# Kernel tuning notes

Measured on AMD Instinct MI355X. Metric: run time of the kernel, lower is better.

Reference implementation:

```python
import jax, jax.numpy as jnp
import numpy as np

# dims derived from init_kwargs
B, C, T, F = 16, 2, 16, 256
TP, FP = 4, 4            # time/freq patch
MF = F // FP             # 64 freq tokens
TIC = T // TP            # 4 time tokens per chunk
S = MF * TIC             # 256 tokens per chunk
CTX = 3
LEFT = S * CTX           # 768 cached tokens
MT = TIC * (CTX + 1)     # 16 max time positions
D, H, G = 512, 8, 4      # d_model, q heads, kv groups
HD = D // H              # 64
R = H // G               # 2 q-heads per kv group
L = 4                    # layers
FFH = 4 * D
EPS = 1e-5


def _ln(x, g, b):
    m = jnp.mean(x, -1, keepdims=True)
    v = jnp.mean((x - m) ** 2, -1, keepdims=True)
    return (x - m) * jax.lax.rsqrt(v + EPS) * g + b


def setup_inputs() -> dict:
    key = jax.random.key(0)
    ks = iter(jax.random.split(key, 20))
    rn = lambda shape, s=0.05: jax.random.normal(next(ks), shape, jnp.float32) * s
    return {
        "x": rn((B, C, T, F), 1.0),
        "cache_k": rn((L, B, G, LEFT, HD), 1.0),
        "cache_v": rn((L, B, G, LEFT, HD), 1.0),
        "in_W": rn((TP * FP * C, D)), "in_b": jnp.zeros((D,)),
        "ln1_g": jnp.ones((L, D)), "ln1_b": jnp.zeros((L, D)),
        "Wq": rn((L, D, D)), "bq": jnp.zeros((L, D)),
        "Wk": rn((L, D, G * HD)), "bk": jnp.zeros((L, G * HD)),
        "Wv": rn((L, D, G * HD)), "bv": jnp.zeros((L, G * HD)),
        "Wo": rn((L, D, D)), "bo": jnp.zeros((L, D)),
        "rel_time": rn((L, 2 * MT - 1, H)), "rel_freq": rn((L, 2 * MF - 1, H)),
        "res_a": jnp.ones((L,)),
        "ln2_g": jnp.ones((L, D)), "ln2_b": jnp.zeros((L, D)),
        "W1": rn((L, D, FFH)), "b1": jnp.zeros((L, FFH)),
        "W3": rn((L, D, FFH)), "b3": jnp.zeros((L, FFH)),
        "W2": rn((L, FFH, D)), "b2": jnp.zeros((L, D)),
        "res_f": jnp.ones((L,)),
        "out_W": rn((D, TP * FP * C)), "out_b": jnp.zeros((TP * FP * C,)),
    }


def reference(x, cache_k, cache_v, in_W, in_b, ln1_g, ln1_b, Wq, bq, Wk, bk, Wv, bv,
              Wo, bo, rel_time, rel_freq, res_a, ln2_g, ln2_b, W1, b1, W3, b3, W2, b2,
              res_f, out_W, out_b):
    # patchify: (B,C,T,F) -> (B, S, TP*FP*C), token order time-major / freq inner
    h = jnp.transpose(x, (0, 2, 3, 1)).reshape(B, TIC, TP, MF, FP, C)
    h = jnp.transpose(h, (0, 1, 3, 2, 4, 5)).reshape(B, S, TP * FP * C)
    h = h @ in_W + in_b  # (B,S,D)

    # 2D relative position indices (identical each layer)
    K = LEFT + S
    q_idx = jnp.arange(S)
    k_idx = jnp.arange(K)
    qt = LEFT // MF + q_idx // MF  # query time = cache time offset + local time
    qf = q_idx % MF
    kt = k_idx // MF
    kf = k_idx % MF
    dt = qt[:, None] - kt[None, :] + (MT - 1)  # (S,K) in [0, 2*MT-2]
    df = qf[:, None] - kf[None, :] + (MF - 1)  # (S,K) in [0, 2*MF-2]
    scale = 1.0 / np.sqrt(HD).astype(np.float32)

    new_ck, new_cv = [], []
    for l in range(L):
        # --- streaming GQA attention with 2D rel-pos and KV cache ---
        xin = _ln(h, ln1_g[l], ln1_b[l])
        q = (xin @ Wq[l] + bq[l]).reshape(B, S, H, HD)
        k = (xin @ Wk[l] + bk[l]).reshape(B, S, G, HD)
        v = (xin @ Wv[l] + bv[l]).reshape(B, S, G, HD)
        k_full = jnp.concatenate([cache_k[l], jnp.transpose(k, (0, 2, 1, 3))], axis=2)  # (B,G,K,HD)
        v_full = jnp.concatenate([cache_v[l], jnp.transpose(v, (0, 2, 1, 3))], axis=2)
        new_ck.append(k_full[:, :, -LEFT:])
        new_cv.append(v_full[:, :, -LEFT:])
        # group q heads: head h -> group h // R
        scores = jnp.einsum('bsgrd,bgtd->bgrst', q.reshape(B, S, G, R, HD), k_full) * scale
        bias = rel_time[l][dt] + rel_freq[l][df]          # (S,K,H)
        bias = jnp.transpose(bias, (2, 0, 1)).reshape(G, R, S, K)
        attn = jax.nn.softmax(scores + bias[None], axis=-1)
        o = jnp.einsum('bgrst,bgtd->bsgrd', attn, v_full).reshape(B, S, D)
        o = o @ Wo[l] + bo[l]
        h = h + res_a[l] * o  # dropout/droppath identity at eval
        # --- SwiGLU FFN ---
        xin = _ln(h, ln2_g[l], ln2_b[l])
        ff = (jax.nn.silu(xin @ W1[l] + b1[l]) * (xin @ W3[l] + b3[l])) @ W2[l] + b2[l]
        h = h + res_f[l] * ff

    y = h @ out_W + out_b  # (B,S,TP*FP*C)
    # unpatchify back to (B,C,T,F)
    y = y.reshape(B, TIC, MF, TP, FP, C)
    y = jnp.transpose(y, (0, 1, 3, 2, 4, 5)).reshape(B, T, F, C)
    y = jnp.transpose(y, (0, 3, 1, 2))
    return y, jnp.stack(new_ck), jnp.stack(new_cv)
```

## Files before the change

### kernel.cpp

```cpp
#include <hip/hip_runtime.h>
#include <stdint.h>

typedef __attribute__((ext_vector_type(8))) short bf16x8;
typedef __attribute__((ext_vector_type(4))) float f32x4;

#define B_    16
#define S_    256
#define LEFT_ 768
#define KT_   1024
#define D_    512
#define H_    8
#define G_    4
#define HD_   64
#define L_    4
#define FFH_  2048
#define M_    4096
#define LOG2E 1.44269504f

__device__ __forceinline__ unsigned short f2b(float f){
  unsigned u = __float_as_uint(f);
  u += 0x7fffu + ((u>>16)&1u);
  return (unsigned short)(u>>16);
}

__device__ __forceinline__ void gl_lds16(const unsigned short* g, void* l){
  __builtin_amdgcn_global_load_lds(
    (const __attribute__((address_space(1))) unsigned int*)g,
    (__attribute__((address_space(3))) unsigned int*)l, 16, 0, 0);
}

template<int BM, int BN, int WM, int WN, class BRowF>
__device__ __forceinline__ void mfma_core(
    const unsigned short* Abase, int lda, int m0, BRowF brow,
    int kd, char* As, char* Bs, f32x4* acc)
{
  constexpr int FR = WM/16, FC = WN/16;
  constexpr int NWC = BN/WN;
  constexpr int CA = BM/64, CB = BN/64;
  const int tid = threadIdx.x, wave = tid>>6, lane = tid&63;
  const int wr = wave / NWC, wc = wave % NWC;
  const int lr = lane>>2;
  const int swl = (lane&3) ^ ((lane>>2)&3) ^ (lane>>4);

  auto stage = [&](int buf, int k0){
    #pragma unroll
    for (int i = 0; i < CA; ++i) {
      const int chunk = wave*CA + i;
      const unsigned short* gp = Abase + (size_t)(m0 + chunk*16 + lr)*lda + k0 + swl*8;
      gl_lds16(gp, As + buf*(BM*64) + chunk*1024);
    }
    #pragma unroll
    for (int i = 0; i < CB; ++i) {
      const int chunk = wave*CB + i;
      const unsigned short* gp = brow(chunk*16 + lr) + k0 + swl*8;
      gl_lds16(gp, Bs + buf*(BN*64) + chunk*1024);
    }
  };

  stage(0, 0);
  __syncthreads();
  int cur = 0;
  for (int k0 = 0; k0 < kd; k0 += 32) {
    if (k0 + 32 < kd) stage(cur^1, k0 + 32);
    bf16x8 af[FR], bfr[FC];
    #pragma unroll
    for (int r = 0; r < FR; ++r)
      af[r] = *(const bf16x8*)(As + cur*(BM*64) + (wr*WM + r*16 + (lane&15))*64 + swl*16);
    #pragma unroll
    for (int c = 0; c < FC; ++c)
      bfr[c] = *(const bf16x8*)(Bs + cur*(BN*64) + (wc*WN + c*16 + (lane&15))*64 + swl*16);
    #pragma unroll
    for (int r = 0; r < FR; ++r)
      #pragma unroll
      for (int c = 0; c < FC; ++c)
        acc[r*FC+c] = __builtin_amdgcn_mfma_f32_16x16x32_bf16(af[r], bfr[c], acc[r*FC+c], 0, 0, 0);
    __syncthreads();
    cur ^= 1;
  }
}

__device__ __forceinline__ void tcvt_body(
    const float* __restrict__ src, unsigned short* __restrict__ dst,
    int K, int N, int ntk, int ntn, int bx)
{
  __shared__ float t[64][65];
  int kt = bx % ntk; int nt = (bx/ntk) % ntn; int l = bx/(ntk*ntn);
  src += (size_t)l*K*N; dst += (size_t)l*N*K;
  const int k0 = kt*64, n0 = nt*64;
  const int tid = threadIdx.x;
  #pragma unroll
  for (int i = 0; i < 4; ++i) {
    int kr = (tid>>4) + i*16;
    const float4 v = *(const float4*)&src[(size_t)(k0+kr)*N + n0 + (tid&15)*4];
    t[kr][(tid&15)*4+0]=v.x; t[kr][(tid&15)*4+1]=v.y;
    t[kr][(tid&15)*4+2]=v.z; t[kr][(tid&15)*4+3]=v.w;
  }
  __syncthreads();
  const int nn = tid>>2, kk = (tid&3)*16;
  unsigned w[8];
  #pragma unroll
  for (int j = 0; j < 8; ++j)
    w[j] = (unsigned)f2b(t[kk+2*j][nn]) | ((unsigned)f2b(t[kk+2*j+1][nn])<<16);
  size_t off = (size_t)(n0+nn)*K + k0 + kk;
  *(uint4*)&dst[off]     = make_uint4(w[0],w[1],w[2],w[3]);
  *(uint4*)&dst[off + 8] = make_uint4(w[4],w[5],w[6],w[7]);
}

__global__ __launch_bounds__(256) void transpose_all(
    const float* __restrict__ Wq, const float* __restrict__ Wk,
    const float* __restrict__ Wv, const float* __restrict__ Wo,
    const float* __restrict__ W1, const float* __restrict__ W3,
    const float* __restrict__ W2,
    unsigned short* __restrict__ Wqt, unsigned short* __restrict__ Wkt,
    unsigned short* __restrict__ Wvt, unsigned short* __restrict__ Wot,
    unsigned short* __restrict__ W1t, unsigned short* __restrict__ W3t,
    unsigned short* __restrict__ W2t)
{
  int bx = blockIdx.x;
  if      (bx < 256)  tcvt_body(Wq, Wqt, 512, 512, 8, 8,  bx);
  else if (bx < 384)  tcvt_body(Wk, Wkt, 512, 256, 8, 4,  bx-256);
  else if (bx < 512)  tcvt_body(Wv, Wvt, 512, 256, 8, 4,  bx-384);
  else if (bx < 768)  tcvt_body(Wo, Wot, 512, 512, 8, 8,  bx-512);
  else if (bx < 1792) tcvt_body(W1, W1t, 512, 2048, 8, 32, bx-768);
  else if (bx < 2816) tcvt_body(W3, W3t, 512, 2048, 8, 32, bx-1792);
  else                tcvt_body(W2, W2t, 2048, 512, 32, 8, bx-2816);
}

__global__ __launch_bounds__(256) void patchify_inproj(
    const float* __restrict__ x, const float* __restrict__ inW,
    const float* __restrict__ inb, float* __restrict__ h)
{
  __shared__ float wlds[32*512];
  __shared__ float ps[16][33];
  const int tid = threadIdx.x;
  const int tb = blockIdx.x*16;

  #pragma unroll
  for (int i = 0; i < 16; ++i)
    ((float4*)wlds)[i*256 + tid] = ((const float4*)inW)[i*256 + tid];
  {
    int tok = tid >> 5, idx = tid & 31;
    int bs = tb + tok;
    int b = bs >> 8, s = bs & 255;
    int tic = s >> 6, mf = s & 63;
    int tp = idx >> 3, fp = (idx >> 1) & 3, c = idx & 1;
    ps[tok][idx] = x[((size_t)(b*2 + c)*16 + tic*4 + tp)*256 + mf*4 + fp];
    int tok2 = tok + 8;
    int bs2 = tb + tok2;
    int b2 = bs2 >> 8, s2 = bs2 & 255;
    int tic2 = s2 >> 6, mf2 = s2 & 63;
    ps[tok2][idx] = x[((size_t)(b2*2 + c)*16 + tic2*4 + tp)*256 + mf2*4 + fp];
  }
  __syncthreads();

  const int g = tid >> 4, qd = tid & 15;
  const int bs = tb + g;
  for (int j = 0; j < 32; ++j) {
    int d = j*16 + qd;
    float acc = inb[d];
    #pragma unroll
    for (int i = 0; i < 32; ++i) acc += ps[g][i] * wlds[i*512 + d];
    h[(size_t)bs*512 + d] = acc;
  }
}

__global__ __launch_bounds__(256) void ln_stats(
    const float* __restrict__ h, float* __restrict__ smean, float* __restrict__ srstd)
{
  const int tid = threadIdx.x;
  const int row = blockIdx.x*16 + (tid>>4);
  const int qd = tid & 15;
  const float* rp = h + (size_t)row*512 + qd*32;
  float s = 0.f, sq = 0.f;
  #pragma unroll
  for (int i = 0; i < 8; ++i) {
    float4 v = ((const float4*)rp)[i];
    s  += (v.x+v.y)+(v.z+v.w);
    sq += (v.x*v.x+v.y*v.y)+(v.z*v.z+v.w*v.w);
  }
  #pragma unroll
  for (int o = 1; o < 16; o <<= 1) { s += __shfl_xor(s,o,64); sq += __shfl_xor(sq,o,64); }
  if (qd == 0) {
    float mean = s*(1.f/512.f);
    smean[row] = mean;
    srstd[row] = rsqrtf(sq*(1.f/512.f) - mean*mean + 1e-5f);
  }
}

__global__ __launch_bounds__(256) void ln_kernel(
    const float* __restrict__ in, unsigned short* __restrict__ out,
    const float* __restrict__ g, const float* __restrict__ bta)
{
  const int tid = threadIdx.x;
  const int row = blockIdx.x*16 + (tid>>4);
  const int qd = tid & 15;
  const float* rp = in + (size_t)row*512 + qd*32;
  float4 xv[8];
  float s = 0.f, sq = 0.f;
  #pragma unroll
  for (int i = 0; i < 8; ++i) {
    xv[i] = ((const float4*)rp)[i];
    s  += (xv[i].x+xv[i].y)+(xv[i].z+xv[i].w);
    sq += (xv[i].x*xv[i].x + xv[i].y*xv[i].y)+(xv[i].z*xv[i].z + xv[i].w*xv[i].w);
  }
  #pragma unroll
  for (int o = 1; o < 16; o <<= 1) { s += __shfl_xor(s,o,64); sq += __shfl_xor(sq,o,64); }
  const float mean = s*(1.f/512.f);
  const float rstd = rsqrtf(sq*(1.f/512.f) - mean*mean + 1e-5f);
  const float* gp = g + qd*32;
  const float* bp = bta + qd*32;
  unsigned short* op = out + (size_t)row*512 + qd*32;
  #pragma unroll
  for (int i = 0; i < 4; ++i) {
    float4 a  = xv[2*i],                 b2 = xv[2*i+1];
    float4 ga = ((const float4*)gp)[2*i], gb = ((const float4*)gp)[2*i+1];
    float4 ba = ((const float4*)bp)[2*i], bb = ((const float4*)bp)[2*i+1];
    unsigned w0 = (unsigned)f2b((a.x-mean)*rstd*ga.x + ba.x) | ((unsigned)f2b((a.y-mean)*rstd*ga.y + ba.y)<<16);
    unsigned w1 = (unsigned)f2b((a.z-mean)*rstd*ga.z + ba.z) | ((unsigned)f2b((a.w-mean)*rstd*ga.w + ba.w)<<16);
    unsigned w2 = (unsigned)f2b((b2.x-mean)*rstd*gb.x + bb.x) | ((unsigned)f2b((b2.y-mean)*rstd*gb.y + bb.y)<<16);
    unsigned w3 = (unsigned)f2b((b2.z-mean)*rstd*gb.z + bb.z) | ((unsigned)f2b((b2.w-mean)*rstd*gb.w + bb.w)<<16);
    *(uint4*)(op + i*8) = make_uint4(w0,w1,w2,w3);
  }
}

__global__ __launch_bounds__(256) void qkv_ln_gemm(
    const float* __restrict__ h,
    const float* __restrict__ smean, const float* __restrict__ srstd,
    const float* __restrict__ lng, const float* __restrict__ lnb,
    const unsigned short* __restrict__ Wqt, const unsigned short* __restrict__ Wkt,
    const unsigned short* __restrict__ Wvt,
    const float* __restrict__ bq, const float* __restrict__ bk_, const float* __restrict__ bv_,
    unsigned short* __restrict__ q_bf, unsigned short* __restrict__ kf_bf,
    unsigned short* __restrict__ vnew, float* __restrict__ nck, float* __restrict__ ncv)
{
  __shared__ alignas(16) char As[2][64*64];
  __shared__ alignas(16) char Bs[2][128*64];
  int bx = (blockIdx.x & 7)*64 + (blockIdx.x >> 3);
  const int mt = bx >> 3, nt = bx & 7;
  const int m0 = mt*64, n0 = nt*128;
  const int tid = threadIdx.x, wave = tid>>6, lane = tid&63;

  const int ar = tid >> 2, au = tid & 3;
  const int ap = au ^ (ar&3) ^ ((ar>>2)&3);
  const float* arow = h + (size_t)(m0 + ar)*512;
  const float mean_r = smean[m0 + ar];
  const float rstd_r = srstd[m0 + ar];

  const int lr = lane>>2;
  const int swl = (lane&3) ^ ((lane>>2)&3) ^ (lane>>4);
  auto brow = [&](int rr) -> const unsigned short* {
    int n = n0 + rr;
    return n < 512 ? Wqt + (size_t)n*512
         : n < 768 ? Wkt + (size_t)(n-512)*512
                   : Wvt + (size_t)(n-768)*512;
  };
  auto stageB = [&](int buf, int k0){
    #pragma unroll
    for (int i = 0; i < 2; ++i) {
      const int chunk = wave*2 + i;
      gl_lds16(brow(chunk*16+lr) + k0 + swl*8, (char*)Bs[buf] + chunk*1024);
    }
  };

  float4 av[6];
  auto loadA = [&](int k0){
    av[0] = *(const float4*)(arow + k0 + au*8);
    av[1] = *(const float4*)(arow + k0 + au*8 + 4);
    av[2] = *(const float4*)(lng  + k0 + au*8);
    av[3] = *(const float4*)(lng  + k0 + au*8 + 4);
    av[4] = *(const float4*)(lnb  + k0 + au*8);
    av[5] = *(const float4*)(lnb  + k0 + au*8 + 4);
  };
  auto writeA = [&](int buf){
    const float* xv = (const float*)&av[0];
    const float* gv = (const float*)&av[2];
    const float* bv2 = (const float*)&av[4];
    unsigned w[4];
    #pragma unroll
    for (int j = 0; j < 4; ++j) {
      float e0 = (xv[2*j]   - mean_r)*rstd_r*gv[2*j]   + bv2[2*j];
      float e1 = (xv[2*j+1] - mean_r)*rstd_r*gv[2*j+1] + bv2[2*j+1];
      w[j] = (unsigned)f2b(e0) | ((unsigned)f2b(e1)<<16);
    }
    *(uint4*)((char*)As[buf] + ar*64 + ap*16) = make_uint4(w[0],w[1],w[2],w[3]);
  };

  loadA(0);
  stageB(0, 0);
  writeA(0);
  __syncthreads();

  f32x4 acc[8] = {};
  const int wr = wave >> 1, wc = wave & 1;
  for (int k0 = 0; k0 < 512; k0 += 32) {
    const int cur = (k0>>5)&1;
    const bool more = (k0 + 32 < 512);
    if (more) { stageB(cur^1, k0+32); loadA(k0+32); }
    bf16x8 af[2], bfv[4];
    #pragma unroll
    for (int r = 0; r < 2; ++r)
      af[r] = *(const bf16x8*)((char*)As[cur] + (wr*32 + r*16 + (lane&15))*64 + swl*16);
    #pragma unroll
    for (int c = 0; c < 4; ++c)
      bfv[c] = *(const bf16x8*)((char*)Bs[cur] + (wc*64 + c*16 + (lane&15))*64 + swl*16);
    #pragma unroll
    for (int r = 0; r < 2; ++r)
      #pragma unroll
      for (int c = 0; c < 4; ++c)
        acc[r*4+c] = __builtin_amdgcn_mfma_f32_16x16x32_bf16(af[r], bfv[c], acc[r*4+c], 0,0,0);
    if (more) writeA(cur^1);
    __syncthreads();
  }

  #pragma unroll
  for (int r = 0; r < 2; ++r)
  #pragma unroll
  for (int c = 0; c < 4; ++c) {
    f32x4 v = acc[r*4+c];
    #pragma unroll
    for (int reg = 0; reg < 4; ++reg) {
      int m = m0 + wr*32 + r*16 + ((lane>>4)<<2) + reg;
      int n = n0 + wc*64 + c*16 + (lane&15);
      float val = v[reg];
      int b = m >> 8, s = m & 255;
      if (n < 512) {
        q_bf[(size_t)m*512 + n] = f2b(val + bq[n]);
      } else if (n < 768) {
        int g = (n-512) >> 6, hd = n & 63;
        float kv = val + bk_[n-512];
        kf_bf[((size_t)(b*4+g)*1024 + 768 + s)*64 + hd] = f2b(kv);
        nck [((size_t)(b*4+g)*768  + 512 + s)*64 + hd] = kv;
      } else {
        int g = (n-768) >> 6, hd = n & 63;
        float vv = val + bv_[n-768];
        vnew[(size_t)m*256 + (n-768)] = f2b(vv);
        ncv [((size_t)(b*4+g)*768 + 512 + s)*64 + hd] = vv;
      }
    }
  }
}

__global__ __launch_bounds__(256) void merge_kv(
    const float* __restrict__ ck, const float* __restrict__ cv,
    const unsigned short* __restrict__ vnew,
    unsigned short* __restrict__ kf_bf, unsigned short* __restrict__ vt_bf,
    float* __restrict__ nck, float* __restrict__ ncv)
{
  __shared__ float t[64][65];
  const int bb = blockIdx.x;
  const int tid = threadIdx.x;
  if (bb < 3072) {
    size_t idx = (size_t)bb*256 + tid;
    int hd4 = idx & 15;
    size_t tt = (idx >> 4) % 768;
    size_t bg = idx / (16*768);
    const float4 v = ((const float4*)ck)[idx];
    uint2 pk;
    pk.x = (unsigned)f2b(v.x) | ((unsigned)f2b(v.y)<<16);
    pk.y = (unsigned)f2b(v.z) | ((unsigned)f2b(v.w)<<16);
    *(uint2*)&kf_bf[((bg*1024 + tt)*64) + hd4*4] = pk;
    if (tt >= 256)
      ((float4*)nck)[(bg*768 + (tt-256))*16 + hd4] = v;
  } else if (bb < 3840) {
    const int bi = bb - 3072;
    const int bg = bi / 12, tt = bi % 12;
    const int t0 = tt*64;
    #pragma unroll
    for (int i = 0; i < 4; ++i) {
      int tr = (tid>>4) + i*16;
      const float4 v = ((const float4*)cv)[((size_t)bg*768 + t0+tr)*16 + (tid&15)];
      t[tr][(tid&15)*4+0]=v.x; t[tr][(tid&15)*4+1]=v.y;
      t[tr][(tid&15)*4+2]=v.z; t[tr][(tid&15)*4+3]=v.w;
      if (t0+tr >= 256)
        ((float4*)ncv)[((size_t)bg*768 + t0+tr-256)*16 + (tid&15)] = v;
    }
    __syncthreads();
    const int hd = tid>>2, tc = (tid&3)*16;
    unsigned w[8];
    #pragma unroll
    for (int j = 0; j < 8; ++j)
      w[j] = (unsigned)f2b(t[tc+2*j][hd]) | ((unsigned)f2b(t[tc+2*j+1][hd])<<16);
    size_t off = ((size_t)bg*64 + hd)*1024 + t0 + tc;
    *(uint4*)&vt_bf[off]     = make_uint4(w[0],w[1],w[2],w[3]);
    *(uint4*)&vt_bf[off + 8] = make_uint4(w[4],w[5],w[6],w[7]);
  } else {
    const int bi = bb - 3840;
    const int bg = bi >> 2, tt4 = bi & 3;
    const int b = bg >> 2, g = bg & 3;
    const int t0 = 768 + tt4*64;
    unsigned short* ts = (unsigned short*)&t[0][0];
    #pragma unroll
    for (int i = 0; i < 4; ++i) {
      int tr = (tid>>4) + i*16;
      uint2 v = *(const uint2*)&vnew[((size_t)(b*256 + (t0-768) + tr))*256 + g*64 + (tid&15)*4];
      const unsigned short* pv4 = (const unsigned short*)&v;
      ts[tr*68 + (tid&15)*4 + 0] = pv4[0];
      ts[tr*68 + (tid&15)*4 + 1] = pv4[1];
      ts[tr*68 + (tid&15)*4 + 2] = pv4[2];
      ts[tr*68 + (tid&15)*4 + 3] = pv4[3];
    }
    __syncthreads();
    const int hd = tid>>2, tc = (tid&3)*16;
    unsigned w[8];
    #pragma unroll
    for (int j = 0; j < 8; ++j)
      w[j] = (unsigned)ts[(tc+2*j)*68 + hd] | ((unsigned)ts[(tc+2*j+1)*68 + hd] << 16);
    size_t off = ((size_t)bg*64 + hd)*1024 + t0 + tc;
    *(uint4*)&vt_bf[off]     = make_uint4(w[0],w[1],w[2],w[3]);
    *(uint4*)&vt_bf[off + 8] = make_uint4(w[4],w[5],w[6],w[7]);
  }
}

__global__ __launch_bounds__(512) void flash_attn(
    const unsigned short* __restrict__ q_bf,
    const unsigned short* __restrict__ kf_bf,
    const unsigned short* __restrict__ vt_bf,
    const float* __restrict__ relt,
    const float* __restrict__ relf,
    unsigned short* __restrict__ att_bf)
{
  int bx = (blockIdx.x & 7)*32 + (blockIdx.x >> 3);
  const int qt = bx & 1, hh = (bx>>1) & 7, b = bx >> 4;
  const int g = hh >> 1;
  const int tid = threadIdx.x, wave = tid>>6, lane = tid&63;
  const int lg = lane>>4, lq = lane&15;
  const int qloc = wave*16 + lq;
  const int q0 = qt*128;
  const int qtg = qt*2 + (wave>>2);

  __shared__ alignas(16) char Ks[2][16384];
  __shared__ alignas(16) char Vs[2][16384];

  const unsigned short* kfb  = kf_bf + (size_t)(b*4+g)*1024*64;
  const unsigned short* vtb2 = vt_bf + (size_t)(b*4+g)*64*1024;

  auto stage = [&](int buf, int t){
    #pragma unroll
    for (int it = 0; it < 2; ++it) {
      int slot = it*512 + tid;
      int kr = slot>>3, kp = slot&7,  ku = kp ^ (kr&7);
      gl_lds16(kfb + (size_t)(t*128 + kr)*64 + ku*8, Ks[buf] + slot*16);
      int vr = slot>>4, vp = slot&15, vu = vp ^ (vr&15);
      gl_lds16(vtb2 + (size_t)vr*1024 + t*128 + vu*8, Vs[buf] + slot*16);
    }
  };

  const unsigned short* qrow = q_bf + ((size_t)(b*256 + q0 + qloc))*512 + hh*64;
  bf16x8 qfrag[2];
  qfrag[0] = *(const bf16x8*)(qrow + lg*8);
  qfrag[1] = *(const bf16x8*)(qrow + 32 + lg*8);

  float bias_f[4][4];
  {
    int sq = qloc & 63;
    #pragma unroll
    for (int f = 0; f < 4; ++f)
      #pragma unroll
      for (int r = 0; r < 4; ++r)
        bias_f[f][r] = relf[((sq - (f*16 + lg*4 + r)) + 63)*8 + hh] * LOG2E;
  }
  const float scale2 = 0.125f * LOG2E;

  f32x4 ot[4] = {};
  float m_run = -1e30f, l_part = 0.f;

  stage(0, 0);
  __syncthreads();

  for (int t = 0; t < 8; ++t) {
    const int cur = t & 1;
    if (t + 1 < 8) stage(cur^1, t+1);

    f32x4 st[8] = {};
    __builtin_amdgcn_s_setprio(1);
    #pragma unroll
    for (int c = 0; c < 2; ++c)
      #pragma unroll
      for (int f = 0; f < 8; ++f) {
        int row = f*16 + lq;
        int pu = (c*4 + lg) ^ (row & 7);
        bf16x8 kf_ = *(const bf16x8*)(Ks[cur] + row*128 + pu*16);
        st[f] = __builtin_amdgcn_mfma_f32_16x16x32_bf16(kf_, qfrag[c], st[f], 0,0,0);
      }
    __builtin_amdgcn_s_setprio(0);

    const float bt0 = relt[(27 + qtg - 2*t)*8 + hh] * LOG2E;
    const float bt1 = relt[(27 + qtg - 2*t - 1)*8 + hh] * LOG2E;
    float mt = -1e30f;
    #pragma unroll
    for (int f = 0; f < 8; ++f) {
      const float bt = (f < 4) ? bt0 : bt1;
      #pragma unroll
      for (int r = 0; r < 4; ++r) {
        float v = st[f][r]*scale2 + bt + bias_f[f&3][r];
        st[f][r] = v;
        mt = fmaxf(mt, v);
      }
    }
    mt = fmaxf(mt, __shfl_xor(mt, 16, 64));
    mt = fmaxf(mt, __shfl_xor(mt, 32, 64));
    if (!__all(mt - m_run <= 11.5416f)) {
      const float m_new = fmaxf(m_run, mt);
      const float corr = exp2f(m_run - m_new);
      m_run = m_new;
      l_part *= corr;
      #pragma unroll
      for (int f = 0; f < 4; ++f) {
        ot[f][0] *= corr; ot[f][1] *= corr; ot[f][2] *= corr; ot[f][3] *= corr;
      }
    }
    float psum = 0.f;
    unsigned r01[8], r23[8];
    #pragma unroll
    for (int f = 0; f < 8; ++f) {
      float e0 = exp2f(st[f][0] - m_run);
      float e1 = exp2f(st[f][1] - m_run);
      float e2 = exp2f(st[f][2] - m_run);
      float e3 = exp2f(st[f][3] - m_run);
      psum += (e0+e1)+(e2+e3);
      r01[f] = (unsigned)f2b(e0) | ((unsigned)f2b(e1)<<16);
      r23[f] = (unsigned)f2b(e2) | ((unsigned)f2b(e3)<<16);
    }
    l_part += psum;

    const int src0 = (lg&1)*32 + lq;
    const int src1 = src0 + 16;
    const bool hi = (lg>>1) != 0;
    #pragma unroll
    for (int c = 0; c < 4; ++c) {
      unsigned a0 = (unsigned)__shfl((int)r01[c*2],   src0, 64);
      unsigned b0 = (unsigned)__shfl((int)r01[c*2+1], src0, 64);
      unsigned a1 = (unsigned)__shfl((int)r23[c*2],   src0, 64);
      unsigned b1 = (unsigned)__shfl((int)r23[c*2+1], src0, 64);
      unsigned a2 = (unsigned)__shfl((int)r01[c*2],   src1, 64);
      unsigned b2 = (unsigned)__shfl((int)r01[c*2+1], src1, 64);
      unsigned a3 = (unsigned)__shfl((int)r23[c*2],   src1, 64);
      unsigned b3 = (unsigned)__shfl((int)r23[c*2+1], src1, 64);
      uint4 bw;
      bw.x = hi ? b0 : a0;
      bw.y = hi ? b1 : a1;
      bw.z = hi ? b2 : a2;
      bw.w = hi ? b3 : a3;
      bf16x8 pfrag = *(bf16x8*)&bw;
      __builtin_amdgcn_s_setprio(1);
      #pragma unroll
      for (int f = 0; f < 4; ++f) {
        int row = f*16 + lq;
        int pu = (c*4 + lg) ^ (row & 15);
        bf16x8 vf_ = *(const bf16x8*)(Vs[cur] + row*256 + pu*16);
        ot[f] = __builtin_amdgcn_mfma_f32_16x16x32_bf16(vf_, pfrag, ot[f], 0,0,0);
      }
      __builtin_amdgcn_s_setprio(0);
    }
    __syncthreads();
  }

  float l_tot = l_part + __shfl_xor(l_part, 16, 64);
  l_tot += __shfl_xor(l_tot, 32, 64);
  const float inv = 1.0f / l_tot;
  unsigned short* orow = att_bf + ((size_t)(b*256 + q0 + qloc))*512 + hh*64;
  #pragma unroll
  for (int f = 0; f < 4; ++f) {
    uint2 w;
    w.x = (unsigned)f2b(ot[f][0]*inv) | ((unsigned)f2b(ot[f][1]*inv)<<16);
    w.y = (unsigned)f2b(ot[f][2]*inv) | ((unsigned)f2b(ot[f][3]*inv)<<16);
    *(uint2*)(orow + f*16 + lg*4) = w;
  }
}

__global__ __launch_bounds__(256) void ffn1_gemm(
    const unsigned short* __restrict__ xin,
    const unsigned short* __restrict__ W1t, const unsigned short* __restrict__ W3t,
    const float* __restrict__ b1_, const float* __restrict__ b3_,
    unsigned short* __restrict__ ff_bf)
{
  __shared__ alignas(16) char As[2*128*64];
  __shared__ alignas(16) char Bs[2*128*64];
  f32x4 acc[16] = {};
  int bx = (blockIdx.x & 7)*128 + (blockIdx.x >> 3);
  const int nt = bx & 31, mt = bx >> 5;
  const int m0 = mt*128, n0 = nt*128;
  auto brow = [&](int r) -> const unsigned short* {
    int p = n0 + r;
    int pb = p >> 4;
    int j = ((pb>>1)<<4) | (p & 15);
    return (pb & 1) ? W3t + (size_t)j*512 : W1t + (size_t)j*512;
  };
  mfma_core<128,128,64,64>(xin, 512, m0, brow, 512, As, Bs, acc);
  const int lane = threadIdx.x & 63, wave = threadIdx.x >> 6;
  const int wr = wave >> 1, wc = wave & 1;
  #pragma unroll
  for (int r = 0; r < 4; ++r)
  #pragma unroll
  for (int cp = 0; cp < 4; cp += 2) {
    f32x4 va = acc[r*4+cp];
    f32x4 vb = acc[r*4+cp+1];
    #pragma unroll
    for (int reg = 0; reg < 4; ++reg) {
      int m = m0 + wr*64 + r*16 + ((lane>>4)<<2) + reg;
      int p = n0 + wc*64 + cp*16 + (lane&15);
      int j = ((p>>5)<<4) | (p & 15);
      float a = va[reg] + b1_[j];
      float bb = vb[reg] + b3_[j];
      float gval = (a / (1.0f + __expf(-a))) * bb;
      ff_bf[(size_t)m*2048 + j] = f2b(gval);
    }
  }
}

__global__ __launch_bounds__(256) void res_gemm(
    const unsigned short* __restrict__ A, int lda,
    const unsigned short* __restrict__ Wt, int kd,
    const float* __restrict__ bias, const float* __restrict__ resv,
    float* __restrict__ h)
{
  __shared__ alignas(16) char As[4][64*64];
  __shared__ alignas(16) char Bs[4][64*64];
  f32x4 acc[4] = {};
  int bx = (blockIdx.x & 7)*64 + (blockIdx.x >> 3);
  const int mt = bx >> 3, nt = bx & 7;
  const int m0 = mt*64, n0 = nt*64;
  const int tid = threadIdx.x, wave = tid>>6, lane = tid&63;
  const int wr = wave >> 1, wc = wave & 1;
  const int lr = lane>>2;
  const int swl = (lane&3) ^ ((lane>>2)&3) ^ (lane>>4);

  auto stageP = [&](int slot, int k0){
    gl_lds16(A  + (size_t)(m0 + wave*16 + lr)*lda + k0 + swl*8, As[slot] + wave*1024);
    gl_lds16(Wt + (size_t)(n0 + wave*16 + lr)*kd  + k0 + swl*8, Bs[slot] + wave*1024);
  };

  stageP(0, 0);
  stageP(1, 32);
  __syncthreads();
  int cur = 0;
  for (int k0 = 0; k0 < kd; k0 += 64) {
    if (k0 + 64 < kd) { stageP((cur^1)*2, k0+64); stageP((cur^1)*2+1, k0+96); }
    #pragma unroll
    for (int p = 0; p < 2; ++p) {
      const char* ab = As[cur*2+p];
      const char* bb = Bs[cur*2+p];
      bf16x8 af[2], bfv[2];
      #pragma unroll
      for (int r = 0; r < 2; ++r)
        af[r] = *(const bf16x8*)(ab + (wr*32 + r*16 + (lane&15))*64 + swl*16);
      #pragma unroll
      for (int c = 0; c < 2; ++c)
        bfv[c] = *(const bf16x8*)(bb + (wc*32 + c*16 + (lane&15))*64 + swl*16);
      #pragma unroll
      for (int r = 0; r < 2; ++r)
        #pragma unroll
        for (int c = 0; c < 2; ++c)
          acc[r*2+c] = __builtin_amdgcn_mfma_f32_16x16x32_bf16(af[r], bfv[c], acc[r*2+c], 0,0,0);
    }
    __syncthreads();
    cur ^= 1;
  }

  const float rv = resv[0];
  #pragma unroll
  for (int r = 0; r < 2; ++r)
  #pragma unroll
  for (int c = 0; c < 2; ++c) {
    f32x4 v = acc[r*2+c];
    #pragma unroll
    for (int reg = 0; reg < 4; ++reg) {
      int m = m0 + wr*32 + r*16 + ((lane>>4)<<2) + reg;
      int n = n0 + wc*32 + c*16 + (lane&15);
      h[(size_t)m*512 + n] += rv * (v[reg] + bias[n]);
    }
  }
}

__global__ __launch_bounds__(256) void outproj_kernel(
    const float* __restrict__ h, const float* __restrict__ outW,
    const float* __restrict__ outb, float* __restrict__ y)
{
  int bs = blockIdx.x;
  int b = bs >> 8, s = bs & 255;
  int tic = s >> 6, mf = s & 63;
  __shared__ float hr[512];
  __shared__ float part[8][32];
  int tid = threadIdx.x;
  hr[tid]     = h[(size_t)bs*D_ + tid];
  hr[tid+256] = h[(size_t)bs*D_ + tid + 256];
  __syncthreads();
  int i = tid & 31, seg = tid >> 5;
  float acc = 0.0f;
  #pragma unroll
  for (int k = 0; k < 64; ++k) acc += hr[seg*64 + k] * outW[(seg*64 + k)*32 + i];
  part[seg][i] = acc;
  __syncthreads();
  if (tid < 32) {
    float v = outb[tid];
    #pragma unroll
    for (int s2 = 0; s2 < 8; ++s2) v += part[s2][tid];
    int tp = tid >> 3, fp = (tid >> 1) & 3, c = tid & 1;
    y[((size_t)(b*2 + c)*16 + tic*4 + tp)*256 + mf*4 + fp] = v;
  }
}

extern "C" void kernel_launch(void* const* d_in, const int* in_sizes, int n_in,
                              void* d_out, int out_size, void* d_ws, size_t ws_size,
                              hipStream_t stream) {
  (void)in_sizes; (void)n_in; (void)out_size; (void)ws_size;
  const float* x        = (const float*)d_in[0];
  const float* cache_k  = (const float*)d_in[1];
  const float* cache_v  = (const float*)d_in[2];
  const float* in_W     = (const float*)d_in[3];
  const float* in_b     = (const float*)d_in[4];
  const float* ln1_g    = (const float*)d_in[5];
  const float* ln1_b    = (const float*)d_in[6];
  const float* Wq       = (const float*)d_in[7];
  const float* bq       = (const float*)d_in[8];
  const float* Wk       = (const float*)d_in[9];
  const float* bk       = (const float*)d_in[10];
  const float* Wv       = (const float*)d_in[11];
  const float* bv       = (const float*)d_in[12];
  const float* Wo       = (const float*)d_in[13];
  const float* bo       = (const float*)d_in[14];
  const float* rel_time = (const float*)d_in[15];
  const float* rel_freq = (const float*)d_in[16];
  const float* res_a    = (const float*)d_in[17];
  const float* ln2_g    = (const float*)d_in[18];
  const float* ln2_b    = (const float*)d_in[19];
  const float* W1       = (const float*)d_in[20];
  const float* b1       = (const float*)d_in[21];
  const float* W3       = (const float*)d_in[22];
  const float* b3       = (const float*)d_in[23];
  const float* W2       = (const float*)d_in[24];
  const float* b2       = (const float*)d_in[25];
  const float* res_f    = (const float*)d_in[26];
  const float* out_W    = (const float*)d_in[27];
  const float* out_b    = (const float*)d_in[28];

  char* ws = (char*)d_ws;
  size_t o = 0;
  float* h            = (float*)(ws + o);          o += (size_t)4096*512*4;
  unsigned short* xin = (unsigned short*)(ws + o); o += (size_t)4096*512*2;
  unsigned short* qb  = (unsigned short*)(ws + o); o += (size_t)4096*512*2;
  unsigned short* att = (unsigned short*)(ws + o); o += (size_t)4096*512*2;
  unsigned short* kfb = (unsigned short*)(ws + o); o += (size_t)64*1024*64*2;
  unsigned short* vtb = (unsigned short*)(ws + o); o += (size_t)64*64*1024*2;
  unsigned short* vnw = (unsigned short*)(ws + o); o += (size_t)4096*256*2;
  float* smean        = (float*)(ws + o);          o += (size_t)4096*4;
  float* srstd        = (float*)(ws + o);          o += (size_t)4096*4;
  unsigned short* Wqt = (unsigned short*)(ws + o); o += (size_t)4*512*512*2;
  unsigned short* Wkt = (unsigned short*)(ws + o); o += (size_t)4*256*512*2;
  unsigned short* Wvt = (unsigned short*)(ws + o); o += (size_t)4*256*512*2;
  unsigned short* Wot = (unsigned short*)(ws + o); o += (size_t)4*512*512*2;
  unsigned short* W1t = (unsigned short*)(ws + o); o += (size_t)4*2048*512*2;
  unsigned short* W3t = (unsigned short*)(ws + o); o += (size_t)4*2048*512*2;
  unsigned short* W2t = (unsigned short*)(ws + o); o += (size_t)4*512*2048*2;
  unsigned short* ffb = (unsigned short*)(ws + o);

  float* y    = (float*)d_out;
  float* nck0 = y + 131072;
  float* ncv0 = nck0 + 12582912;

  transpose_all<<<3840, 256, 0, stream>>>(Wq, Wk, Wv, Wo, W1, W3, W2,
                                          Wqt, Wkt, Wvt, Wot, W1t, W3t, W2t);

  patchify_inproj<<<256, 256, 0, stream>>>(x, in_W, in_b, h);

  for (int l = 0; l < L_; ++l) {
    ln_stats<<<256, 256, 0, stream>>>(h, smean, srstd);
    qkv_ln_gemm<<<512, 256, 0, stream>>>(
        h, smean, srstd, ln1_g + l*512, ln1_b + l*512,
        Wqt + (size_t)l*512*512, Wkt + (size_t)l*256*512, Wvt + (size_t)l*256*512,
        bq + l*512, bk + l*256, bv + l*256,
        qb, kfb, vnw, nck0 + (size_t)l*3145728, ncv0 + (size_t)l*3145728);
    merge_kv<<<4096, 256, 0, stream>>>(
        cache_k + (size_t)l*3145728, cache_v + (size_t)l*3145728, vnw,
        kfb, vtb, nck0 + (size_t)l*3145728, ncv0 + (size_t)l*3145728);
    flash_attn<<<256, 512, 0, stream>>>(qb, kfb, vtb,
        rel_time + l*31*8, rel_freq + l*127*8, att);
    res_gemm<<<512, 256, 0, stream>>>(att, 512, Wot + (size_t)l*512*512, 512,
                                      bo + l*512, res_a + l, h);
    ln_kernel<<<256, 256, 0, stream>>>(h, xin, ln2_g + l*512, ln2_b + l*512);
    ffn1_gemm<<<1024, 256, 0, stream>>>(
        xin, W1t + (size_t)l*2048*512, W3t + (size_t)l*2048*512,
        b1 + l*2048, b3 + l*2048, ffb);
    res_gemm<<<512, 256, 0, stream>>>(ffb, 2048, W2t + (size_t)l*512*2048, 2048,
                                      b2 + l*512, res_f + l, h);
  }

  outproj_kernel<<<M_, 256, 0, stream>>>(h, out_W, out_b, y);
}
```

Before: 602.3 us.

## Deepen QKV GEMM pipeline to four LDS stages and batch output projection tokens

The fused LN+QKV GEMM now uses four LDS slots and processes two k-steps per barrier. This halves the number of __syncthreads calls and gives the loads more time to overlap with the MFMAs, at the cost of twice the shared memory, which may lower occupancy. The output projection kernel now handles 8 tokens per block, stages the full out_W matrix in LDS once per block, and launches 512 blocks instead of 4096. This removes the cross-segment reduction and cuts redundant weight reads from global memory.

Result: no change. 609.5 us (+1.2%).

```diff
diff --git a/kernel.cpp b/kernel.cpp
--- a/kernel.cpp
+++ b/kernel.cpp
@@ -233,8 +233,8 @@
     unsigned short* __restrict__ q_bf, unsigned short* __restrict__ kf_bf,
     unsigned short* __restrict__ vnew, float* __restrict__ nck, float* __restrict__ ncv)
 {
-  __shared__ alignas(16) char As[2][64*64];
-  __shared__ alignas(16) char Bs[2][128*64];
+  __shared__ alignas(16) char As[4][64*64];
+  __shared__ alignas(16) char Bs[4][128*64];
   int bx = (blockIdx.x & 7)*64 + (blockIdx.x >> 3);
   const int mt = bx >> 3, nt = bx & 7;
   const int m0 = mt*64, n0 = nt*128;
@@ -254,11 +254,11 @@
          : n < 768 ? Wkt + (size_t)(n-512)*512
                    : Wvt + (size_t)(n-768)*512;
   };
-  auto stageB = [&](int buf, int k0){
+  auto stageB = [&](int slot, int k0){
     #pragma unroll
     for (int i = 0; i < 2; ++i) {
       const int chunk = wave*2 + i;
-      gl_lds16(brow(chunk*16+lr) + k0 + swl*8, (char*)Bs[buf] + chunk*1024);
+      gl_lds16(brow(chunk*16+lr) + k0 + swl*8, (char*)Bs[slot] + chunk*1024);
     }
   };
 
@@ -271,7 +271,7 @@
     av[4] = *(const float4*)(lnb  + k0 + au*8);
     av[5] = *(const float4*)(lnb  + k0 + au*8 + 4);
   };
-  auto writeA = [&](int buf){
+  auto writeA = [&](int slot){
     const float* xv = (const float*)&av[0];
     const float* gv = (const float*)&av[2];
     const float* bv2 = (const float*)&av[4];
@@ -282,34 +282,41 @@
       float e1 = (xv[2*j+1] - mean_r)*rstd_r*gv[2*j+1] + bv2[2*j+1];
       w[j] = (unsigned)f2b(e0) | ((unsigned)f2b(e1)<<16);
     }
-    *(uint4*)((char*)As[buf] + ar*64 + ap*16) = make_uint4(w[0],w[1],w[2],w[3]);
+    *(uint4*)((char*)As[slot] + ar*64 + ap*16) = make_uint4(w[0],w[1],w[2],w[3]);
   };
 
-  loadA(0);
-  stageB(0, 0);
-  writeA(0);
+  loadA(0);  stageB(0, 0);  writeA(0);
+  loadA(32); stageB(1, 32); writeA(1);
   __syncthreads();
 
   f32x4 acc[8] = {};
   const int wr = wave >> 1, wc = wave & 1;
-  for (int k0 = 0; k0 < 512; k0 += 32) {
-    const int cur = (k0>>5)&1;
-    const bool more = (k0 + 32 < 512);
-    if (more) { stageB(cur^1, k0+32); loadA(k0+32); }
+
+  auto mfmaP = [&](int slot){
     bf16x8 af[2], bfv[4];
     #pragma unroll
     for (int r = 0; r < 2; ++r)
-      af[r] = *(const bf16x8*)((char*)As[cur] + (wr*32 + r*16 + (lane&15))*64 + swl*16);
+      af[r] = *(const bf16x8*)((char*)As[slot] + (wr*32 + r*16 + (lane&15))*64 + swl*16);
     #pragma unroll
     for (int c = 0; c < 4; ++c)
-      bfv[c] = *(const bf16x8*)((char*)Bs[cur] + (wc*64 + c*16 + (lane&15))*64 + swl*16);
+      bfv[c] = *(const bf16x8*)((char*)Bs[slot] + (wc*64 + c*16 + (lane&15))*64 + swl*16);
     #pragma unroll
     for (int r = 0; r < 2; ++r)
       #pragma unroll
       for (int c = 0; c < 4; ++c)
         acc[r*4+c] = __builtin_amdgcn_mfma_f32_16x16x32_bf16(af[r], bfv[c], acc[r*4+c], 0,0,0);
-    if (more) writeA(cur^1);
+  };
+
+  int cur = 0;
+  for (int k0 = 0; k0 < 512; k0 += 64) {
+    const bool more = (k0 + 64 < 512);
+    if (more) { stageB((cur^1)*2, k0+64); loadA(k0+64); }
+    mfmaP(cur*2);
+    if (more) { writeA((cur^1)*2); stageB((cur^1)*2+1, k0+96); loadA(k0+96); }
+    mfmaP(cur*2+1);
+    if (more) writeA((cur^1)*2+1);
     __syncthreads();
+    cur ^= 1;
   }
 
   #pragma unroll
@@ -676,28 +683,36 @@
     const float* __restrict__ h, const float* __restrict__ outW,
     const float* __restrict__ outb, float* __restrict__ y)
 {
-  int bs = blockIdx.x;
-  int b = bs >> 8, s = bs & 255;
-  int tic = s >> 6, mf = s & 63;
-  __shared__ float hr[512];
-  __shared__ float part[8][32];
-  int tid = threadIdx.x;
-  hr[tid]     = h[(size_t)bs*D_ + tid];
-  hr[tid+256] = h[(size_t)bs*D_ + tid + 256];
+  __shared__ float wlds[512*32];
+  __shared__ float hr[8][520];
+  const int tid = threadIdx.x;
+  const int tb = blockIdx.x*8;
+
+  #pragma unroll
+  for (int i = 0; i < 16; ++i)
+    ((float4*)wlds)[i*256 + tid] = ((const float4*)outW)[i*256 + tid];
+  {
+    const int tok = tid >> 5, idx = tid & 31;
+    const float* hrow = h + (size_t)(tb + tok)*512;
+    #pragma unroll
+    for (int i = 0; i < 4; ++i) {
+      float4 v = ((const float4*)hrow)[idx + i*32];
+      int e = (idx + i*32)*4;
+      hr[tok][e+0] = v.x; hr[tok][e+1] = v.y; hr[tok][e+2] = v.z; hr[tok][e+3] = v.w;
+    }
+  }
   __syncthreads();
-  int i = tid & 31, seg = tid >> 5;
-  float acc = 0.0f;
-  #pragma unroll
-  for (int k = 0; k < 64; ++k) acc += hr[seg*64 + k] * outW[(seg*64 + k)*32 + i];
-  part[seg][i] = acc;
-  __syncthreads();
-  if (tid < 32) {
-    float v = outb[tid];
-    #pragma unroll
-    for (int s2 = 0; s2 < 8; ++s2) v += part[s2][tid];
-    int tp = tid >> 3, fp = (tid >> 1) & 3, c = tid & 1;
-    y[((size_t)(b*2 + c)*16 + tic*4 + tp)*256 + mf*4 + fp] = v;
-  }
+
+  const int tok = tid >> 5, i = tid & 31;
+  float acc = outb[i];
+  #pragma unroll 8
+  for (int k = 0; k < 512; ++k) acc += hr[tok][k] * wlds[k*32 + i];
+
+  const int bs = tb + tok;
+  const int b = bs >> 8, s = bs & 255;
+  const int tic = s >> 6, mf = s & 63;
+  const int tp = i >> 3, fp = (i >> 1) & 3, c = i & 1;
+  y[((size_t)(b*2 + c)*16 + tic*4 + tp)*256 + mf*4 + fp] = acc;
 }
 
 extern "C" void kernel_launch(void* const* d_in, const int* in_sizes, int n_in,
@@ -785,5 +800,5 @@
                                       b2 + l*512, res_f + l, h);
   }
 
-  outproj_kernel<<<M_, 256, 0, stream>>>(h, out_W, out_b, y);
-}
+  outproj_kernel<<<512, 256, 0, stream>>>(h, out_W, out_b, y);
+}
```
